# Kernel tuning notes

Measured on AMD Instinct MI355X. Metric: run time of the kernel, lower is better.

Reference implementation:

```python
import jax, jax.numpy as jnp
import numpy as np

B_, H_, W_ = 4, 64, 64
D_INNER, D_STATE, DT_RANK, K = 192, 16, 6, 4
DT_MIN, DT_MAX = 0.001, 0.1


def setup_inputs() -> dict:
    key = jax.random.key(0)
    ks = jax.random.split(key, 8)
    x = jax.random.normal(ks[0], (B_, D_INNER, H_, W_), dtype=jnp.float32)
    y = jax.random.normal(ks[1], (B_, D_INNER, H_, W_), dtype=jnp.float32)
    # x_proj: 4 stacked Linear(d_inner1 -> dt_rank + 2*d_state) weights
    x_proj_weight = jax.random.normal(ks[2], (K, DT_RANK + 2 * D_STATE, D_INNER), dtype=jnp.float32) * (D_INNER ** -0.5)
    # dt_proj weights: uniform(-dt_rank^-0.5, dt_rank^-0.5)
    s = DT_RANK ** -0.5
    dt_projs_weight = jax.random.uniform(ks[3], (K, D_INNER, DT_RANK), dtype=jnp.float32, minval=-s, maxval=s)
    # dt bias init: inverse softplus of dt ~ loguniform(dt_min, dt_max)
    dt = jnp.exp(jax.random.uniform(ks[4], (K, D_INNER), dtype=jnp.float32)
                 * (np.log(DT_MAX) - np.log(DT_MIN)) + np.log(DT_MIN))
    dt = jnp.clip(dt, 1e-4, None)
    dt_projs_bias = dt + jnp.log(-jnp.expm1(-dt))
    # A_logs: log(1..N) repeated over K*d_inner channels
    A_logs = jnp.tile(jnp.log(jnp.arange(1, D_STATE + 1, dtype=jnp.float32))[None, :], (K * D_INNER, 1))
    Ds = jnp.ones((K * D_INNER,), dtype=jnp.float32)
    ln_gamma = jnp.ones((D_INNER,), dtype=jnp.float32)
    ln_beta = jnp.zeros((D_INNER,), dtype=jnp.float32)
    return {"x": x, "y": y, "x_proj_weight": x_proj_weight, "dt_projs_weight": dt_projs_weight,
            "dt_projs_bias": dt_projs_bias, "A_logs": A_logs, "Ds": Ds,
            "ln_gamma": ln_gamma, "ln_beta": ln_beta}


def _cross_scan(t):
    # (B, C, H, W) -> (B, 4, C, L): [row-major, col-major, and their reverses]
    B, C, H, W = t.shape
    a = t.reshape(B, C, H * W)
    b = jnp.swapaxes(t, 2, 3).reshape(B, C, H * W)
    s = jnp.stack([a, b], axis=1)  # (B,2,C,L)
    return jnp.concatenate([s, jnp.flip(s, axis=-1)], axis=1)  # (B,4,C,L)


def reference(x, y, x_proj_weight, dt_projs_weight, dt_projs_bias, A_logs, Ds, ln_gamma, ln_beta):
    B, C, H, W = x.shape
    L = H * W
    N = A_logs.shape[-1]
    R = dt_projs_weight.shape[-1]
    D = dt_projs_weight.shape[1]

    xs = _cross_scan(x)  # (B,K,C,L)
    ys = _cross_scan(y)  # (B,K,D,L) -- u for the scan

    x_dbl = jnp.einsum('bkdl,kcd->bkcl', xs, x_proj_weight)
    dts, Bs, Cs = x_dbl[:, :, :R], x_dbl[:, :, R:R + N], x_dbl[:, :, R + N:]
    dts = jnp.einsum('bkrl,kdr->bkdl', dts, dt_projs_weight)  # (B,K,D,L)

    delta = jax.nn.softplus(dts + dt_projs_bias.reshape(1, K, D, 1))  # (B,K,D,L)
    A = -jnp.exp(A_logs).reshape(K, D, N)  # (K,D,N)

    # selective scan over L: h_t = exp(delta_t*A)*h_{t-1} + delta_t*B_t*u_t; y_t = C_t . h_t
    u_l = jnp.moveaxis(ys, 3, 0)      # (L,B,K,D)
    d_l = jnp.moveaxis(delta, 3, 0)   # (L,B,K,D)
    B_l = jnp.moveaxis(Bs, 3, 0)      # (L,B,K,N)
    C_l = jnp.moveaxis(Cs, 3, 0)      # (L,B,K,N)

    def step(h, inp):
        u_t, d_t, b_t, c_t = inp
        dA = jnp.exp(d_t[..., None] * A)                       # (B,K,D,N)
        h = dA * h + (d_t * u_t)[..., None] * b_t[:, :, None, :]
        y_t = jnp.einsum('bkdn,bkn->bkd', h, c_t)
        return h, y_t

    h0 = jnp.zeros((B, K, D, N), dtype=jnp.float32)
    _, y_scan = jax.lax.scan(step, h0, (u_l, d_l, B_l, C_l))   # (L,B,K,D)
    out_y = jnp.moveaxis(y_scan, 0, 3) + Ds.reshape(1, K, D, 1) * ys  # (B,K,D,L)

    # cross-merge
    inv_y = jnp.flip(out_y[:, 2:4], axis=-1)                   # (B,2,D,L)
    wh_y = jnp.swapaxes(out_y[:, 1].reshape(B, D, W, H), 2, 3).reshape(B, D, L)
    invwh_y = jnp.swapaxes(inv_y[:, 1].reshape(B, D, W, H), 2, 3).reshape(B, D, L)
    ya = out_y[:, 0] + inv_y[:, 0] + wh_y + invwh_y            # (B,D,L)

    ya = jnp.swapaxes(ya, 1, 2).reshape(B, H, W, D)
    mu = jnp.mean(ya, axis=-1, keepdims=True)
    var = jnp.var(ya, axis=-1, keepdims=True)
    return (ya - mu) * jax.lax.rsqrt(var + 1e-5) * ln_gamma + ln_beta
```

## Files before the change

### kernel.cpp

```cpp
#include <hip/hip_runtime.h>
#include <hip/hip_bf16.h>

#define BB 4
#define KK 4
#define DD 192
#define NN 16
#define RR 6
#define LL 4096
#define NC 64
#define CL 64
#define C38 38

__device__ __forceinline__ float ex2(float x) {
#if __has_builtin(__builtin_amdgcn_exp2f)
  return __builtin_amdgcn_exp2f(x);
#else
  return exp2f(x);
#endif
}

__global__ __launch_bounds__(256) void k_trans(
    const float* __restrict__ x, const float* __restrict__ y,
    float* __restrict__ xT, float* __restrict__ yT)
{
  __shared__ float t0l[64 * 65];
  __shared__ float t1l[64 * 65];
  const int tid = threadIdx.x;
  const int ti = tid & 63;
  const int r4 = tid >> 6;
  const int mm0 = blockIdx.x * 2;
  const int mm1 = mm0 + 1;
  const float* s0 = (mm0 < 768 ? x + (size_t)mm0 * 4096 : y + (size_t)(mm0 - 768) * 4096);
  const float* s1 = (mm1 < 768 ? x + (size_t)mm1 * 4096 : y + (size_t)(mm1 - 768) * 4096);
  float* d0 = (mm0 < 768 ? xT + (size_t)mm0 * 4096 : yT + (size_t)(mm0 - 768) * 4096);
  float* d1 = (mm1 < 768 ? xT + (size_t)mm1 * 4096 : yT + (size_t)(mm1 - 768) * 4096);
#pragma unroll
  for (int r = r4; r < 64; r += 4) t0l[r * 65 + ti] = s0[r * 64 + ti];
#pragma unroll
  for (int r = r4; r < 64; r += 4) t1l[r * 65 + ti] = s1[r * 64 + ti];
  __syncthreads();
#pragma unroll
  for (int r = r4; r < 64; r += 4) d0[r * 64 + ti] = t0l[ti * 65 + r];
#pragma unroll
  for (int r = r4; r < 64; r += 4) d1[r * 64 + ti] = t1l[ti * 65 + r];
}

__global__ __launch_bounds__(256) void k_proj(
    const float* __restrict__ x, const float* __restrict__ xT,
    const float* __restrict__ y, const float* __restrict__ yT,
    const float* __restrict__ xpw, const float* __restrict__ dpw,
    const float* __restrict__ dpb,
    float* __restrict__ delta_ws, float* __restrict__ u_ws,
    float* __restrict__ bs_ws, float* __restrict__ cs_ws)
{
  __shared__ float xs[64 * 65];
  __shared__ float xd[38 * 65];
  const int bid = blockIdx.x;
  const int tile = bid & 63;
  const int k = (bid >> 6) & 3;
  const int b = bid >> 8;
  const int tid = threadIdx.x;
  const int ti = tid & 63;
  const int ds4 = tid >> 6;
  const int wv = __builtin_amdgcn_readfirstlane(ds4);

  const int m = (k >= 2) ? (4095 - tile * 64 - ti) : (tile * 64 + ti);
  const size_t bkL = (size_t)(b * KK + k) * LL;
  const size_t rowbase = bkL + tile * 64;
  const float* xb = ((k & 1) ? xT : x) + (size_t)b * DD * LL;

  const int c0 = (wv == 3) ? 28 : wv * 10;
  const float* Wk = xpw + (size_t)k * C38 * DD;
  float acc[10];
#pragma unroll
  for (int j = 0; j < 10; ++j) acc[j] = 0.f;
  for (int ch = 0; ch < 3; ++ch) {
    for (int r = ds4; r < 64; r += 4)
      xs[r * 65 + ti] = xb[(size_t)(ch * 64 + r) * LL + m];
    __syncthreads();
    const float* Wc = Wk + ch * 64;
#pragma unroll 8
    for (int dj = 0; dj < 64; ++dj) {
      float xv = xs[dj * 65 + ti];
#pragma unroll
      for (int j = 0; j < 10; ++j)
        acc[j] = fmaf(xv, Wc[(c0 + j) * DD + dj], acc[j]);
    }
    __syncthreads();
  }
#pragma unroll
  for (int j = 0; j < 10; ++j) xd[(c0 + j) * 65 + ti] = acc[j];
  __syncthreads();

  for (int idx = tid; idx < 64 * NN; idx += 256) {
    int i = idx >> 4, n = idx & 15;
    size_t row = rowbase + i;
    bs_ws[row * NN + n] = xd[(RR + n) * 65 + i];
    cs_ws[row * NN + n] = xd[(RR + NN + n) * 65 + i];
  }

  const float* dpwk = dpw + (size_t)k * DD * RR;
  const float* dpbk = dpb + (size_t)k * DD;
  for (int ch = 0; ch < 3; ++ch) {
    float v[16];
#pragma unroll
    for (int q = 0; q < 16; ++q) {
      const int dd2 = ch * 64 + wv * 16 + q;
      float s = dpbk[dd2];
#pragma unroll
      for (int r = 0; r < RR; ++r)
        s = fmaf(xd[r * 65 + ti], dpwk[dd2 * RR + r], s);
      v[q] = (s > 20.f) ? s : __logf(1.f + __expf(s));
    }
    __syncthreads();
#pragma unroll
    for (int q = 0; q < 16; ++q) xs[ti * 65 + wv * 16 + q] = v[q];
    __syncthreads();
    float* dbase = delta_ws + rowbase * DD + ch * 64;
#pragma unroll
    for (int it = 0; it < 16; ++it) {
      const int i = it * 4 + ds4;
      dbase[(size_t)i * DD + ti] = xs[i * 65 + ti];
    }
  }

  if (k < 2) {
    const float* yb = ((k & 1) ? yT : y) + (size_t)b * DD * LL;
    const size_t urowbase = (size_t)(b * 2 + k) * LL + tile * 64;
    for (int ch = 0; ch < 3; ++ch) {
      __syncthreads();
      for (int r = ds4; r < 64; r += 4)
        xs[r * 65 + ti] = yb[(size_t)(ch * 64 + r) * LL + m];
      __syncthreads();
      float* ubase = u_ws + urowbase * DD + ch * 64;
#pragma unroll
      for (int it = 0; it < 16; ++it) {
        const int i = it * 4 + ds4;
        ubase[(size_t)i * DD + ti] = xs[ti * 65 + i];
      }
    }
  }
}

__global__ __launch_bounds__(384) void k_scan1(
    const float* __restrict__ delta_ws, const float* __restrict__ u_ws,
    const float* __restrict__ bs_ws, const float* __restrict__ A_logs,
    float* __restrict__ cP, float* __restrict__ cS)
{
  __shared__ float Bl[CL * NN];
  const int bid = blockIdx.x;
  const int c = bid & (NC - 1);
  const int bk = bid >> 6;
  const int k = bk & 3;
  const int b = bk >> 2;
  const int tid = threadIdx.x;
  const int d = tid >> 1, nh = tid & 1;
  if (c == NC - 1) return;
  const int t0 = c * CL;

  float A2[8];
  const float* al = A_logs + (size_t)(k * DD + d) * NN + nh * 8;
#pragma unroll
  for (int n = 0; n < 8; ++n) A2[n] = -__expf(al[n]) * 1.4426950408889634f;

  const float* bsrc = bs_ws + ((size_t)bk * LL + t0) * NN;
  for (int i = tid; i < CL * NN; i += 384) Bl[i] = bsrc[i];
  __syncthreads();

  const float* dptr = delta_ws + ((size_t)bk * LL + t0) * DD + d;
  const int rev = k >> 1;
  const float* uptr = u_ws +
      ((size_t)(b * 2 + (k & 1)) * LL + (rev ? (LL - 1 - t0) : t0)) * DD + d;
  const int ustep = rev ? -DD : DD;

  float h[8];
#pragma unroll
  for (int n = 0; n < 8; ++n) h[n] = 0.f;
  float dsum = 0.f;
  float de0 = dptr[0], uu0 = uptr[0];
  float de1 = dptr[DD], uu1 = uptr[ustep];
#pragma unroll 2
  for (int t = 0; t < CL; ++t) {
    float de2 = dptr[(t + 2) * DD];
    float uu2 = uptr[(t + 2) * ustep];
    float du = de0 * uu0;
    dsum += de0;
    const float4* bq = (const float4*)(Bl + t * NN + nh * 8);
    float4 b0 = bq[0], b1 = bq[1];
    const float bb[8] = {b0.x,b0.y,b0.z,b0.w, b1.x,b1.y,b1.z,b1.w};
#pragma unroll
    for (int n = 0; n < 8; ++n)
      h[n] = fmaf(ex2(de0 * A2[n]), h[n], du * bb[n]);
    de0 = de1; uu0 = uu1; de1 = de2; uu1 = uu2;
  }
  float* pp = cP + (((size_t)bk * NC + c) * DD + d) * NN + nh * 8;
  float* sp = cS + (((size_t)bk * NC + c) * DD + d) * NN + nh * 8;
#pragma unroll
  for (int n = 0; n < 8; ++n) { pp[n] = ex2(dsum * A2[n]); sp[n] = h[n]; }
}

__global__ __launch_bounds__(256) void k_prefix(
    float* __restrict__ cP, const float* __restrict__ cS)
{
  const int tidg = blockIdx.x * 256 + threadIdx.x;
  const int bk = tidg / (DD * NN);
  const int e = tidg - bk * (DD * NN);
  const size_t base = (size_t)bk * NC * DD * NN + e;
  const int STRIDE = DD * NN;
  float h = 0.f;
  int c = 0;
  for (; c + 4 <= NC - 1; c += 4) {
    float p0 = cP[base + (size_t)(c + 0) * STRIDE];
    float p1 = cP[base + (size_t)(c + 1) * STRIDE];
    float p2 = cP[base + (size_t)(c + 2) * STRIDE];
    float p3 = cP[base + (size_t)(c + 3) * STRIDE];
    float s0 = cS[base + (size_t)(c + 0) * STRIDE];
    float s1 = cS[base + (size_t)(c + 1) * STRIDE];
    float s2 = cS[base + (size_t)(c + 2) * STRIDE];
    float s3 = cS[base + (size_t)(c + 3) * STRIDE];
    h = fmaf(p0, h, s0); cP[base + (size_t)(c + 0) * STRIDE] = h;
    h = fmaf(p1, h, s1); cP[base + (size_t)(c + 1) * STRIDE] = h;
    h = fmaf(p2, h, s2); cP[base + (size_t)(c + 2) * STRIDE] = h;
    h = fmaf(p3, h, s3); cP[base + (size_t)(c + 3) * STRIDE] = h;
  }
  for (; c < NC - 1; ++c) {
    float p = cP[base + (size_t)c * STRIDE];
    float s = cS[base + (size_t)c * STRIDE];
    h = fmaf(p, h, s);
    cP[base + (size_t)c * STRIDE] = h;
  }
}

__global__ __launch_bounds__(384) void k_scan2(
    float* __restrict__ dy_ws,
    const float* __restrict__ u_ws,
    const float* __restrict__ bs_ws, const float* __restrict__ cs_ws,
    const float* __restrict__ A_logs, const float* __restrict__ Ds,
    const float* __restrict__ cHin)
{
  __shared__ float Bl[CL * NN];
  __shared__ float Cl2[CL * NN];
  const int bid = blockIdx.x;
  const int c = bid & (NC - 1);
  const int bk = bid >> 6;
  const int k = bk & 3;
  const int b = bk >> 2;
  const int tid = threadIdx.x;
  const int d = tid >> 1, nh = tid & 1;
  const int t0 = c * CL;

  float A2[8];
  const float* al = A_logs + (size_t)(k * DD + d) * NN + nh * 8;
#pragma unroll
  for (int n = 0; n < 8; ++n) A2[n] = -__expf(al[n]) * 1.4426950408889634f;
  const float Dkd = Ds[k * DD + d];

  float h[8];
  if (c == 0) {
#pragma unroll
    for (int n = 0; n < 8; ++n) h[n] = 0.f;
  } else {
    const float4* hq = (const float4*)(cHin +
        (((size_t)bk * NC + (c - 1)) * DD + d) * NN + nh * 8);
    float4 h0 = hq[0], h1 = hq[1];
    h[0]=h0.x; h[1]=h0.y; h[2]=h0.z; h[3]=h0.w;
    h[4]=h1.x; h[5]=h1.y; h[6]=h1.z; h[7]=h1.w;
  }

  const float* bsrc = bs_ws + ((size_t)bk * LL + t0) * NN;
  const float* csrc = cs_ws + ((size_t)bk * LL + t0) * NN;
  for (int i = tid; i < CL * NN; i += 384) {
    Bl[i] = bsrc[i];
    Cl2[i] = csrc[i];
  }
  __syncthreads();

  float* dyp = dy_ws + ((size_t)bk * LL + t0) * DD + d;
  const int rev = k >> 1;
  const float* uptr = u_ws +
      ((size_t)(b * 2 + (k & 1)) * LL + (rev ? (LL - 1 - t0) : t0)) * DD + d;
  const int ustep = rev ? -DD : DD;

  float de0 = dyp[0], uu0 = uptr[0];
  float de1 = dyp[DD], uu1 = uptr[ustep];
#pragma unroll 2
  for (int t = 0; t < CL; ++t) {
    float de2 = dyp[(t + 2) * DD];
    float uu2 = uptr[(t + 2) * ustep];
    float du = de0 * uu0;
    const float4* bq = (const float4*)(Bl + t * NN + nh * 8);
    const float4* cq = (const float4*)(Cl2 + t * NN + nh * 8);
    float4 b0 = bq[0], b1 = bq[1];
    float4 c0 = cq[0], c1 = cq[1];
    const float bb[8] = {b0.x,b0.y,b0.z,b0.w, b1.x,b1.y,b1.z,b1.w};
    const float cc[8] = {c0.x,c0.y,c0.z,c0.w, c1.x,c1.y,c1.z,c1.w};
    float yv = 0.f;
#pragma unroll
    for (int n = 0; n < 8; ++n) {
      h[n] = fmaf(ex2(de0 * A2[n]), h[n], du * bb[n]);
      yv = fmaf(h[n], cc[n], yv);
    }
    yv += __shfl_xor(yv, 1, 64);
    if (nh == 0) dyp[t * DD] = fmaf(Dkd, uu0, yv);
    de0 = de1; uu0 = uu1; de1 = de2; uu1 = uu2;
  }
}

__global__ __launch_bounds__(256) void k_comb(
    const float* __restrict__ ybuf, const float* __restrict__ gamma,
    const float* __restrict__ beta, float* __restrict__ out)
{
  const int lane = threadIdx.x & 63;
  const int gl = blockIdx.x * 4 + (threadIdx.x >> 6);
  const int b = gl >> 12;
  const int l = gl & 4095;
  const int hh = l >> 6, ww = l & 63;
  const int lt = ww * 64 + hh;
  const size_t base = (size_t)b * KK * LL * DD;
  const float* y0 = ybuf + base + (size_t)(0 * LL + l) * DD;
  const float* y1 = ybuf + base + (size_t)(1 * LL + lt) * DD;
  const float* y2 = ybuf + base + (size_t)(2 * LL + (4095 - l)) * DD;
  const float* y3 = ybuf + base + (size_t)(3 * LL + (4095 - lt)) * DD;

  float s[3];
  float sum = 0.f, sq = 0.f;
#pragma unroll
  for (int j = 0; j < 3; ++j) {
    int d = lane + j * 64;
    float v = y0[d] + y1[d] + y2[d] + y3[d];
    s[j] = v; sum += v; sq = fmaf(v, v, sq);
  }
#pragma unroll
  for (int o = 1; o < 64; o <<= 1) {
    sum += __shfl_xor(sum, o, 64);
    sq  += __shfl_xor(sq, o, 64);
  }
  const float mu = sum * (1.f / 192.f);
  const float var = sq * (1.f / 192.f) - mu * mu;
  const float inv = rsqrtf(var + 1e-5f);
  float* op = out + (size_t)gl * DD;
#pragma unroll
  for (int j = 0; j < 3; ++j) {
    int d = lane + j * 64;
    op[d] = (s[j] - mu) * inv * gamma[d] + beta[d];
  }
}

extern "C" void kernel_launch(void* const* d_in, const int* in_sizes, int n_in,
                              void* d_out, int out_size, void* d_ws, size_t ws_size,
                              hipStream_t stream) {
  const float* x     = (const float*)d_in[0];
  const float* y     = (const float*)d_in[1];
  const float* xpw   = (const float*)d_in[2];
  const float* dpw   = (const float*)d_in[3];
  const float* dpb   = (const float*)d_in[4];
  const float* alogs = (const float*)d_in[5];
  const float* ds    = (const float*)d_in[6];
  const float* gamma = (const float*)d_in[7];
  const float* beta  = (const float*)d_in[8];
  float* w = (float*)d_ws;

  float* delta = w;
  float* u     = w + 12582912;
  float* bs    = w + 18874368;
  float* cs    = w + 19922944;
  float* cP    = w + 20971520;
  float* cS    = w + 24117248;
  float* xT    = cP;
  float* yT    = cS;

  k_trans<<<768, 256, 0, stream>>>(x, y, xT, yT);
  k_proj<<<1024, 256, 0, stream>>>(x, xT, y, yT, xpw, dpw, dpb, delta, u, bs, cs);
  k_scan1<<<1024, 384, 0, stream>>>(delta, u, bs, alogs, cP, cS);
  k_prefix<<<192, 256, 0, stream>>>(cP, cS);
  k_scan2<<<1024, 384, 0, stream>>>(delta, u, bs, cs, alogs, ds, cP);
  k_comb<<<4096, 256, 0, stream>>>(delta, gamma, beta, (float*)d_out);
}
```

Before: 239.1 us.

## Split projection blocks into two halves and deepen scan input prefetch

Each k_proj tile is now handled by two blocks. One computes the dt-rank and B channels, then runs the delta projection. The other computes the C channels and does the u transpose. This doubles the block count, reduces per-thread accumulators and balances work, at the cost of loading each x tile twice. Separately, both scan kernels now prefetch delta and u eight steps ahead in a register ring instead of two, to hide global load latency. This uses more registers and reads further past each chunk's end.

```diff
diff --git a/kernel.cpp b/kernel.cpp
--- a/kernel.cpp
+++ b/kernel.cpp
@@ -54,11 +54,12 @@
     float* __restrict__ bs_ws, float* __restrict__ cs_ws)
 {
   __shared__ float xs[64 * 65];
-  __shared__ float xd[38 * 65];
+  __shared__ float xd[22 * 65];
   const int bid = blockIdx.x;
-  const int tile = bid & 63;
-  const int k = (bid >> 6) & 3;
-  const int b = bid >> 8;
+  const int half = bid & 1;
+  const int tile = (bid >> 1) & 63;
+  const int k = (bid >> 7) & 3;
+  const int b = bid >> 9;
   const int tid = threadIdx.x;
   const int ti = tid & 63;
   const int ds4 = tid >> 6;
@@ -69,74 +70,93 @@
   const size_t rowbase = bkL + tile * 64;
   const float* xb = ((k & 1) ? xT : x) + (size_t)b * DD * LL;
 
-  const int c0 = (wv == 3) ? 28 : wv * 10;
+  const int c0 = (half == 0) ? ((wv == 3) ? 16 : wv * 6) : (22 + wv * 4);
   const float* Wk = xpw + (size_t)k * C38 * DD;
-  float acc[10];
-#pragma unroll
-  for (int j = 0; j < 10; ++j) acc[j] = 0.f;
+  float acc[6];
+#pragma unroll
+  for (int j = 0; j < 6; ++j) acc[j] = 0.f;
+
   for (int ch = 0; ch < 3; ++ch) {
     for (int r = ds4; r < 64; r += 4)
       xs[r * 65 + ti] = xb[(size_t)(ch * 64 + r) * LL + m];
     __syncthreads();
     const float* Wc = Wk + ch * 64;
+    if (half == 0) {
 #pragma unroll 8
-    for (int dj = 0; dj < 64; ++dj) {
-      float xv = xs[dj * 65 + ti];
-#pragma unroll
-      for (int j = 0; j < 10; ++j)
-        acc[j] = fmaf(xv, Wc[(c0 + j) * DD + dj], acc[j]);
+      for (int dj = 0; dj < 64; ++dj) {
+        float xv = xs[dj * 65 + ti];
+#pragma unroll
+        for (int j = 0; j < 6; ++j)
+          acc[j] = fmaf(xv, Wc[(c0 + j) * DD + dj], acc[j]);
+      }
+    } else {
+#pragma unroll 8
+      for (int dj = 0; dj < 64; ++dj) {
+        float xv = xs[dj * 65 + ti];
+#pragma unroll
+        for (int j = 0; j < 4; ++j)
+          acc[j] = fmaf(xv, Wc[(c0 + j) * DD + dj], acc[j]);
+      }
     }
     __syncthreads();
   }
-#pragma unroll
-  for (int j = 0; j < 10; ++j) xd[(c0 + j) * 65 + ti] = acc[j];
+  if (half == 0) {
+#pragma unroll
+    for (int j = 0; j < 6; ++j) xd[(c0 + j) * 65 + ti] = acc[j];
+  } else {
+#pragma unroll
+    for (int j = 0; j < 4; ++j) xd[(c0 - 22 + j) * 65 + ti] = acc[j];
+  }
   __syncthreads();
 
-  for (int idx = tid; idx < 64 * NN; idx += 256) {
-    int i = idx >> 4, n = idx & 15;
-    size_t row = rowbase + i;
-    bs_ws[row * NN + n] = xd[(RR + n) * 65 + i];
-    cs_ws[row * NN + n] = xd[(RR + NN + n) * 65 + i];
-  }
-
-  const float* dpwk = dpw + (size_t)k * DD * RR;
-  const float* dpbk = dpb + (size_t)k * DD;
-  for (int ch = 0; ch < 3; ++ch) {
-    float v[16];
-#pragma unroll
-    for (int q = 0; q < 16; ++q) {
-      const int dd2 = ch * 64 + wv * 16 + q;
-      float s = dpbk[dd2];
-#pragma unroll
-      for (int r = 0; r < RR; ++r)
-        s = fmaf(xd[r * 65 + ti], dpwk[dd2 * RR + r], s);
-      v[q] = (s > 20.f) ? s : __logf(1.f + __expf(s));
-    }
-    __syncthreads();
-#pragma unroll
-    for (int q = 0; q < 16; ++q) xs[ti * 65 + wv * 16 + q] = v[q];
-    __syncthreads();
-    float* dbase = delta_ws + rowbase * DD + ch * 64;
-#pragma unroll
-    for (int it = 0; it < 16; ++it) {
-      const int i = it * 4 + ds4;
-      dbase[(size_t)i * DD + ti] = xs[i * 65 + ti];
-    }
-  }
-
-  if (k < 2) {
-    const float* yb = ((k & 1) ? yT : y) + (size_t)b * DD * LL;
-    const size_t urowbase = (size_t)(b * 2 + k) * LL + tile * 64;
+  if (half == 0) {
+    for (int idx = tid; idx < 64 * NN; idx += 256) {
+      int i = idx >> 4, n = idx & 15;
+      bs_ws[(rowbase + i) * NN + n] = xd[(RR + n) * 65 + i];
+    }
+    const float* dpwk = dpw + (size_t)k * DD * RR;
+    const float* dpbk = dpb + (size_t)k * DD;
     for (int ch = 0; ch < 3; ++ch) {
+      float v[16];
+#pragma unroll
+      for (int q = 0; q < 16; ++q) {
+        const int dd2 = ch * 64 + wv * 16 + q;
+        float s = dpbk[dd2];
+#pragma unroll
+        for (int r = 0; r < RR; ++r)
+          s = fmaf(xd[r * 65 + ti], dpwk[dd2 * RR + r], s);
+        v[q] = (s > 20.f) ? s : __logf(1.f + __expf(s));
+      }
       __syncthreads();
-      for (int r = ds4; r < 64; r += 4)
-        xs[r * 65 + ti] = yb[(size_t)(ch * 64 + r) * LL + m];
+#pragma unroll
+      for (int q = 0; q < 16; ++q) xs[ti * 65 + wv * 16 + q] = v[q];
       __syncthreads();
-      float* ubase = u_ws + urowbase * DD + ch * 64;
+      float* dbase = delta_ws + rowbase * DD + ch * 64;
 #pragma unroll
       for (int it = 0; it < 16; ++it) {
         const int i = it * 4 + ds4;
-        ubase[(size_t)i * DD + ti] = xs[ti * 65 + i];
+        dbase[(size_t)i * DD + ti] = xs[i * 65 + ti];
+      }
+    }
+  } else {
+    for (int idx = tid; idx < 64 * NN; idx += 256) {
+      int i = idx >> 4, n = idx & 15;
+      cs_ws[(rowbase + i) * NN + n] = xd[n * 65 + i];
+    }
+    if (k < 2) {
+      const float* yb = ((k & 1) ? yT : y) + (size_t)b * DD * LL;
+      const size_t urowbase = (size_t)(b * 2 + k) * LL + tile * 64;
+      for (int ch = 0; ch < 3; ++ch) {
+        __syncthreads();
+        for (int r = ds4; r < 64; r += 4)
+          xs[r * 65 + ti] = yb[(size_t)(ch * 64 + r) * LL + m];
+        __syncthreads();
+        float* ubase = u_ws + urowbase * DD + ch * 64;
+#pragma unroll
+        for (int it = 0; it < 16; ++it) {
+          const int i = it * 4 + ds4;
+          ubase[(size_t)i * DD + ti] = xs[ti * 65 + i];
+        }
       }
     }
   }
@@ -177,21 +197,25 @@
 #pragma unroll
   for (int n = 0; n < 8; ++n) h[n] = 0.f;
   float dsum = 0.f;
-  float de0 = dptr[0], uu0 = uptr[0];
-  float de1 = dptr[DD], uu1 = uptr[ustep];
-#pragma unroll 2
-  for (int t = 0; t < CL; ++t) {
-    float de2 = dptr[(t + 2) * DD];
-    float uu2 = uptr[(t + 2) * ustep];
-    float du = de0 * uu0;
-    dsum += de0;
-    const float4* bq = (const float4*)(Bl + t * NN + nh * 8);
-    float4 b0 = bq[0], b1 = bq[1];
-    const float bb[8] = {b0.x,b0.y,b0.z,b0.w, b1.x,b1.y,b1.z,b1.w};
-#pragma unroll
-    for (int n = 0; n < 8; ++n)
-      h[n] = fmaf(ex2(de0 * A2[n]), h[n], du * bb[n]);
-    de0 = de1; uu0 = uu1; de1 = de2; uu1 = uu2;
+  float de[8], uu[8];
+#pragma unroll
+  for (int j = 0; j < 8; ++j) { de[j] = dptr[j * DD]; uu[j] = uptr[j * ustep]; }
+  for (int t8 = 0; t8 < CL; t8 += 8) {
+#pragma unroll
+    for (int j = 0; j < 8; ++j) {
+      const int t = t8 + j;
+      const float dcur = de[j], ucur = uu[j];
+      de[j] = dptr[(t + 8) * DD];
+      uu[j] = uptr[(t + 8) * ustep];
+      const float du = dcur * ucur;
+      dsum += dcur;
+      const float4* bq = (const float4*)(Bl + t * NN + nh * 8);
+      float4 b0 = bq[0], b1 = bq[1];
+      const float bb[8] = {b0.x,b0.y,b0.z,b0.w, b1.x,b1.y,b1.z,b1.w};
+#pragma unroll
+      for (int n = 0; n < 8; ++n)
+        h[n] = fmaf(ex2(dcur * A2[n]), h[n], du * bb[n]);
+    }
   }
   float* pp = cP + (((size_t)bk * NC + c) * DD + d) * NN + nh * 8;
   float* sp = cS + (((size_t)bk * NC + c) * DD + d) * NN + nh * 8;
@@ -281,28 +305,32 @@
       ((size_t)(b * 2 + (k & 1)) * LL + (rev ? (LL - 1 - t0) : t0)) * DD + d;
   const int ustep = rev ? -DD : DD;
 
-  float de0 = dyp[0], uu0 = uptr[0];
-  float de1 = dyp[DD], uu1 = uptr[ustep];
-#pragma unroll 2
-  for (int t = 0; t < CL; ++t) {
-    float de2 = dyp[(t + 2) * DD];
-    float uu2 = uptr[(t + 2) * ustep];
-    float du = de0 * uu0;
-    const float4* bq = (const float4*)(Bl + t * NN + nh * 8);
-    const float4* cq = (const float4*)(Cl2 + t * NN + nh * 8);
-    float4 b0 = bq[0], b1 = bq[1];
-    float4 c0 = cq[0], c1 = cq[1];
-    const float bb[8] = {b0.x,b0.y,b0.z,b0.w, b1.x,b1.y,b1.z,b1.w};
-    const float cc[8] = {c0.x,c0.y,c0.z,c0.w, c1.x,c1.y,c1.z,c1.w};
-    float yv = 0.f;
-#pragma unroll
-    for (int n = 0; n < 8; ++n) {
-      h[n] = fmaf(ex2(de0 * A2[n]), h[n], du * bb[n]);
-      yv = fmaf(h[n], cc[n], yv);
-    }
-    yv += __shfl_xor(yv, 1, 64);
-    if (nh == 0) dyp[t * DD] = fmaf(Dkd, uu0, yv);
-    de0 = de1; uu0 = uu1; de1 = de2; uu1 = uu2;
+  float de[8], uu[8];
+#pragma unroll
+  for (int j = 0; j < 8; ++j) { de[j] = dyp[j * DD]; uu[j] = uptr[j * ustep]; }
+  for (int t8 = 0; t8 < CL; t8 += 8) {
+#pragma unroll
+    for (int j = 0; j < 8; ++j) {
+      const int t = t8 + j;
+      const float dcur = de[j], ucur = uu[j];
+      de[j] = dyp[(t + 8) * DD];
+      uu[j] = uptr[(t + 8) * ustep];
+      const float du = dcur * ucur;
+      const float4* bq = (const float4*)(Bl + t * NN + nh * 8);
+      const float4* cq = (const float4*)(Cl2 + t * NN + nh * 8);
+      float4 b0 = bq[0], b1 = bq[1];
+      float4 c0 = cq[0], c1 = cq[1];
+      const float bb[8] = {b0.x,b0.y,b0.z,b0.w, b1.x,b1.y,b1.z,b1.w};
+      const float cc[8] = {c0.x,c0.y,c0.z,c0.w, c1.x,c1.y,c1.z,c1.w};
+      float yv = 0.f;
+#pragma unroll
+      for (int n = 0; n < 8; ++n) {
+        h[n] = fmaf(ex2(dcur * A2[n]), h[n], du * bb[n]);
+        yv = fmaf(h[n], cc[n], yv);
+      }
+      yv += __shfl_xor(yv, 1, 64);
+      if (nh == 0) dyp[t * DD] = fmaf(Dkd, ucur, yv);
+    }
   }
 }
 
@@ -370,7 +398,7 @@
   float* yT    = cS;
 
   k_trans<<<768, 256, 0, stream>>>(x, y, xT, yT);
-  k_proj<<<1024, 256, 0, stream>>>(x, xT, y, yT, xpw, dpw, dpb, delta, u, bs, cs);
+  k_proj<<<2048, 256, 0, stream>>>(x, xT, y, yT, xpw, dpw, dpb, delta, u, bs, cs);
   k_scan1<<<1024, 384, 0, stream>>>(delta, u, bs, alogs, cP, cS);
   k_prefix<<<192, 256, 0, stream>>>(cP, cS);
   k_scan2<<<1024, 384, 0, stream>>>(delta, u, bs, cs, alogs, ds, cP);
```

Result: slower. 260.5 us (+8.9%).
